# Kernel optimization log

Measured on AMD Instinct MI355X. Metric: run time of the kernel, lower is better.

The kernel has to match this reference:

```python
import jax, jax.numpy as jnp
import numpy as np

UNITS = 1024
OUT_STEPS = 200
SEQ_LEN = 5
NUM_FEATURES = 1
BATCH = 4096


def _lstm_cell(x, h, c, kernel, recurrent_kernel, bias):
    # Keras LSTMCell: z = x@K + h@R + b, gates in order i, f, g(candidate), o
    z = x @ kernel + h @ recurrent_kernel + bias  # [B, 4U]
    i, f, g, o = jnp.split(z, 4, axis=-1)
    i = jax.nn.sigmoid(i)
    f = jax.nn.sigmoid(f)
    g = jnp.tanh(g)
    o = jax.nn.sigmoid(o)
    c_new = f * c + i * g
    h_new = o * jnp.tanh(c_new)
    return h_new, c_new


def setup_inputs() -> dict:
    key = jax.random.key(0)
    ks = jax.random.split(key, 8)
    s = 0.05  # modest init scale to keep gates unsaturated
    return {
        "inputs": jax.random.normal(ks[0], (BATCH, SEQ_LEN, NUM_FEATURES), jnp.float32),
        "kernel": jax.random.normal(ks[1], (NUM_FEATURES, 4 * UNITS), jnp.float32) * s,
        "recurrent_kernel": jax.random.normal(ks[2], (UNITS, 4 * UNITS), jnp.float32) * s,
        "bias": jax.random.normal(ks[3], (4 * UNITS,), jnp.float32) * s,
        "w1": jax.random.normal(ks[4], (UNITS, NUM_FEATURES), jnp.float32) * s,
        "b1": jax.random.normal(ks[5], (NUM_FEATURES,), jnp.float32) * s,
        "w2": jax.random.normal(ks[6], (NUM_FEATURES, NUM_FEATURES), jnp.float32) * s,
        "b2": jax.random.normal(ks[7], (NUM_FEATURES,), jnp.float32) * s,
    }


def reference(inputs, kernel, recurrent_kernel, bias, w1, b1, w2, b2):
    B = inputs.shape[0]
    h0 = jnp.zeros((B, UNITS), inputs.dtype)
    c0 = jnp.zeros((B, UNITS), inputs.dtype)

    # warmup: run LSTM over the input sequence (lax.scan over time)
    def warm_step(carry, x_t):
        h, c = carry
        h, c = _lstm_cell(x_t, h, c, kernel, recurrent_kernel, bias)
        return (h, c), None

    (h, c), _ = jax.lax.scan(warm_step, (h0, c0), jnp.swapaxes(inputs, 0, 1))
    pred0 = jax.nn.relu(h @ w1 + b1)  # first prediction: dense1 only (per warmup())

    def dec_step(carry, _):
        pred, h, c = carry
        h, c = _lstm_cell(pred, h, c, kernel, recurrent_kernel, bias)
        x = jax.nn.relu(h @ w1 + b1)
        pred = x @ w2 + b2
        return (pred, h, c), pred

    _, preds = jax.lax.scan(dec_step, (pred0, h, c), None, length=OUT_STEPS - 1)
    # preds: [T-1, B, F] -> stack with pred0 and transpose to [B, T, F]
    all_preds = jnp.concatenate([pred0[None], preds], axis=0)
    return jnp.transpose(all_preds, (1, 0, 2))
```

## Files before the change

### kernel.cpp

```cpp
#include <hip/hip_runtime.h>
#include <hip/hip_bf16.h>
#include <stdint.h>
#include <stddef.h>

#define B_SZ   4096
#define U_SZ   1024
#define SEQ    5
#define TSTEPS 200
#define STEPS  204

typedef __bf16 bf16_t;
typedef __bf16 bf16x8 __attribute__((ext_vector_type(8)));
typedef float  f32x4  __attribute__((ext_vector_type(4)));

#define AS1 __attribute__((address_space(1)))
#define AS3 __attribute__((address_space(3)))

#define LOAD_LDS16(gp, lp) \
    __builtin_amdgcn_global_load_lds((const AS1 unsigned int*)(gp), \
                                     (AS3 unsigned int*)(lp), 16, 0, 0)

__device__ __forceinline__ float fsig(float x) {
    return 1.0f / (1.0f + __expf(-x));
}
__device__ __forceinline__ float ftanh(float x) {
    x = fminf(fmaxf(x, -15.0f), 15.0f);
    float e = __expf(2.0f * x);
    return (e - 1.0f) / (e + 1.0f);
}

__global__ void pack_R(const float* __restrict__ R, bf16_t* __restrict__ Rp) {
    int idx = blockIdx.x * 256 + threadIdx.x;
    int e    = idx & 7;
    int slot = (idx >> 3) & 7;
    int c    = (idx >> 6) & 127;
    int kb   = (idx >> 13) & 15;
    int ub   = idx >> 17;
    int g  = (c >> 4) & 3;
    int wc = c >> 6;
    int cl = c & 15;
    int n  = g * 1024 + ub * 32 + wc * 16 + cl;
    int k  = kb * 64 + ((slot ^ (c & 7)) << 3) + e;
    Rp[idx] = (bf16_t)R[(size_t)k * 4096 + n];
}

__global__ __launch_bounds__(256, 2)
void lstm_step(const bf16_t* __restrict__ hin,
               bf16_t* __restrict__ hout,
               float* __restrict__ cst,
               const bf16_t* __restrict__ Rp,
               const float* __restrict__ Wx,
               const float* __restrict__ bias,
               const float* __restrict__ w1,
               const float* __restrict__ b1,
               const float* __restrict__ w2,
               const float* __restrict__ b2,
               const float* __restrict__ inputs,
               float* __restrict__ praw,
               float* __restrict__ out,
               int t)
{
    __shared__ __align__(16) bf16_t lsA[128 * 64];
    __shared__ __align__(16) bf16_t lsB[2][128 * 64];
    __shared__ float lsX[128];

    const int tid  = threadIdx.x;
    const int wave = tid >> 6;
    const int lane = tid & 63;
    const int p    = blockIdx.x;
    const int G    = blockIdx.y;
    const int l15  = lane & 15;
    const int quad = lane >> 4;
    const int rbase = (wave >> 1) * 64;
    const int wc    = wave & 1;

    float*       pr_acc  = praw + (size_t)(t % 3) * B_SZ;
    const float* pr_read = praw + (size_t)((t + 2) % 3) * B_SZ;
    float*       pr_zero = praw + (size_t)((t + 1) % 3) * B_SZ;

    if (tid < 128) {
        int row = G * 128 + tid;
        float x;
        if (t < SEQ) {
            x = inputs[row * SEQ + t];
        } else {
            float x1 = fmaxf(pr_read[row] + b1[0], 0.f);
            x = (t == SEQ) ? x1 : x1 * w2[0] + b2[0];
            if (p == 0) out[(size_t)row * TSTEPS + (t - SEQ)] = x;
        }
        lsX[tid] = x;
        if (p == 0) pr_zero[row] = 0.f;
    }

    f32x4 acc[2][4][4] = {};
    const bf16_t* Ap  = hin + (size_t)G * 128 * U_SZ;
    const bf16_t* Bp0 = Rp + (size_t)(2 * p) * 131072;
    const bf16_t* Bp1 = Bp0 + 131072;

    const int a_kk = (((lane & 7) ^ (lane >> 3)) << 3);

    for (int kb = 0; kb < 16; ++kb) {
        #pragma unroll
        for (int i = 0; i < 4; ++i) {
            int chunk = wave * 4 + i;
            int m  = chunk * 8 + (lane >> 3);
            LOAD_LDS16(Ap + (size_t)m * U_SZ + kb * 64 + a_kk, &lsA[chunk * 512]);
        }
        #pragma unroll
        for (int i = 0; i < 4; ++i) {
            int chunk = wave * 4 + i;
            LOAD_LDS16(Bp0 + (size_t)kb * 8192 + chunk * 512 + lane * 8,
                       &lsB[0][chunk * 512]);
            LOAD_LDS16(Bp1 + (size_t)kb * 8192 + chunk * 512 + lane * 8,
                       &lsB[1][chunk * 512]);
        }
        __syncthreads();

        #pragma unroll
        for (int kh = 0; kh < 2; ++kh) {
            int sw = (((kh * 4 + quad) ^ (lane & 7)) << 3);
            bf16x8 af[4];
            #pragma unroll
            for (int mi = 0; mi < 4; ++mi)
                af[mi] = *(const bf16x8*)&lsA[(rbase + mi * 16 + l15) * 64 + sw];
            #pragma unroll
            for (int T = 0; T < 2; ++T) {
                bf16x8 bfr[4];
                #pragma unroll
                for (int ni = 0; ni < 4; ++ni)
                    bfr[ni] = *(const bf16x8*)
                        &lsB[T][(wc * 64 + ni * 16 + l15) * 64 + sw];
                #pragma unroll
                for (int mi = 0; mi < 4; ++mi)
                    #pragma unroll
                    for (int ni = 0; ni < 4; ++ni)
                        acc[T][mi][ni] = __builtin_amdgcn_mfma_f32_16x16x32_bf16(
                            af[mi], bfr[ni], acc[T][mi][ni], 0, 0, 0);
            }
        }
        __syncthreads();
    }

    int uu[2];
    uu[0] = (2 * p) * 32 + wc * 16 + l15;
    uu[1] = uu[0] + 32;
    float g_b[2][4], g_w[2][4], w1u[2];
    #pragma unroll
    for (int T = 0; T < 2; ++T) {
        #pragma unroll
        for (int g = 0; g < 4; ++g) {
            g_b[T][g] = bias[g * 1024 + uu[T]];
            g_w[T][g] = Wx[g * 1024 + uu[T]];
        }
        w1u[T] = w1[uu[T]];
    }
    const bool do_pred = (t >= SEQ - 1);

    #pragma unroll
    for (int mi = 0; mi < 4; ++mi) {
        #pragma unroll
        for (int r = 0; r < 4; ++r) {
            int rl   = rbase + mi * 16 + quad * 4 + r;
            int brow = G * 128 + rl;
            float xv = lsX[rl];
            float ps = 0.f;
            #pragma unroll
            for (int T = 0; T < 2; ++T) {
                float zi = acc[T][mi][0][r] + g_b[T][0] + xv * g_w[T][0];
                float zf = acc[T][mi][1][r] + g_b[T][1] + xv * g_w[T][1];
                float zg = acc[T][mi][2][r] + g_b[T][2] + xv * g_w[T][2];
                float zo = acc[T][mi][3][r] + g_b[T][3] + xv * g_w[T][3];
                float ig = fsig(zi), fg = fsig(zf);
                float gg = ftanh(zg), og = fsig(zo);
                size_t off = (size_t)brow * U_SZ + uu[T];
                float cn = fg * cst[off] + ig * gg;
                cst[off] = cn;
                float hv = og * ftanh(cn);
                hout[off] = (bf16_t)hv;
                ps += hv * w1u[T];
            }
            if (do_pred) {
                ps += __shfl_xor(ps, 1);
                ps += __shfl_xor(ps, 2);
                ps += __shfl_xor(ps, 4);
                ps += __shfl_xor(ps, 8);
                if (l15 == 0) atomicAdd(&pr_acc[brow], ps);
            }
        }
    }
}

__global__ void pred_final(const float* __restrict__ praw,
                           const float* __restrict__ b1,
                           const float* __restrict__ w2,
                           const float* __restrict__ b2,
                           float* __restrict__ out)
{
    int row = blockIdx.x * 256 + threadIdx.x;
    float x1 = fmaxf(praw[2 * B_SZ + row] + b1[0], 0.f);
    out[(size_t)row * TSTEPS + 199] = x1 * w2[0] + b2[0];
}

extern "C" void kernel_launch(void* const* d_in, const int* in_sizes, int n_in,
                              void* d_out, int out_size, void* d_ws, size_t ws_size,
                              hipStream_t stream) {
    const float* inputs = (const float*)d_in[0];
    const float* Wx     = (const float*)d_in[1];
    const float* R      = (const float*)d_in[2];
    const float* bias   = (const float*)d_in[3];
    const float* w1     = (const float*)d_in[4];
    const float* b1     = (const float*)d_in[5];
    const float* w2     = (const float*)d_in[6];
    const float* b2     = (const float*)d_in[7];
    float* out = (float*)d_out;

    char* ws = (char*)d_ws;
    const size_t RP_BYTES = (size_t)32 * 131072 * 2;
    const size_t H_BYTES  = (size_t)B_SZ * U_SZ * 2;
    const size_t C_BYTES  = (size_t)B_SZ * U_SZ * 4;
    bf16_t* Rp   = (bf16_t*)ws;                ws += RP_BYTES;
    bf16_t* h0   = (bf16_t*)ws;                ws += H_BYTES;
    bf16_t* h1   = (bf16_t*)ws;                ws += H_BYTES;
    float*  cbuf = (float*)ws;                 ws += C_BYTES;
    float*  praw = (float*)ws;                 ws += 3 * B_SZ * 4;
    bf16_t* hb[2] = {h0, h1};

    hipMemsetAsync(h0, 0, H_BYTES, stream);
    hipMemsetAsync(cbuf, 0, C_BYTES, stream);
    hipMemsetAsync(praw, 0, 3 * B_SZ * 4, stream);

    pack_R<<<16384, 256, 0, stream>>>(R, Rp);

    dim3 grid(16, 32);
    int cur = 0;
    for (int t = 0; t < STEPS; ++t) {
        lstm_step<<<grid, 256, 0, stream>>>(hb[cur], hb[1 - cur], cbuf, Rp,
                                            Wx, bias, w1, b1, w2, b2,
                                            inputs, praw, out, t);
        cur ^= 1;
    }
    pred_final<<<16, 256, 0, stream>>>(praw, b1, w2, b2, out);
}
```

Baseline: 8.692 ms.

## Replace per-step launches with persistent cooperative kernel and per-group barriers

Runs all 204 recurrent steps inside one cooperative persistent kernel. Blocks sharing a batch group synchronise through an atomic counter barrier instead of kernel boundaries. The cell state now stays on chip, half in LDS and half in registers, so it no longer round-trips through global memory. The first K-tile of the recurrent weights is prefetched for the next step during the epilogue. This removes per-launch overhead and the c-state traffic, but adds the barrier spin cost and more LDS per block, which may limit occupancy. A fallback to the old multi-launch path is kept.

```diff
diff --git a/kernel.cpp b/kernel.cpp
--- a/kernel.cpp
+++ b/kernel.cpp
@@ -8,6 +8,8 @@
 #define SEQ    5
 #define TSTEPS 200
 #define STEPS  204
+#define NP     16
+#define NG     32
 
 typedef __bf16 bf16_t;
 typedef __bf16 bf16x8 __attribute__((ext_vector_type(8)));
@@ -42,6 +44,194 @@
     int n  = g * 1024 + ub * 32 + wc * 16 + cl;
     int k  = kb * 64 + ((slot ^ (c & 7)) << 3) + e;
     Rp[idx] = (bf16_t)R[(size_t)k * 4096 + n];
+}
+
+__global__ __launch_bounds__(256, 2)
+void lstm_persist(bf16_t* __restrict__ h0,
+                  bf16_t* __restrict__ h1,
+                  const bf16_t* __restrict__ Rp,
+                  const float* __restrict__ Wx,
+                  const float* __restrict__ bias,
+                  const float* __restrict__ w1,
+                  const float* __restrict__ b1,
+                  const float* __restrict__ w2,
+                  const float* __restrict__ b2,
+                  const float* __restrict__ inputs,
+                  float* __restrict__ praw,
+                  float* __restrict__ out,
+                  unsigned int* __restrict__ bar)
+{
+    __shared__ __align__(16) bf16_t lsA[128 * 64];
+    __shared__ __align__(16) bf16_t lsB[2][128 * 64];
+    __shared__ float lsX[128];
+    __shared__ float lsC[128 * 32];
+
+    const int tid  = threadIdx.x;
+    const int wave = tid >> 6;
+    const int lane = tid & 63;
+    const int p    = blockIdx.x;
+    const int G    = blockIdx.y;
+    const int l15  = lane & 15;
+    const int quad = lane >> 4;
+    const int rbase = (wave >> 1) * 64;
+    const int wc    = wave & 1;
+    const int a_kk  = (((lane & 7) ^ (lane >> 3)) << 3);
+
+    const bf16_t* Bp0 = Rp + (size_t)(2 * p) * 131072;
+    const bf16_t* Bp1 = Bp0 + 131072;
+
+    const int uuA[2] = { (2 * p) * 32 + wc * 16 + l15,
+                         (2 * p) * 32 + wc * 16 + l15 + 32 };
+
+    const float b1s = b1[0], w2s = w2[0], b2s = b2[0];
+
+    for (int i = tid; i < 4096; i += 256) lsC[i] = 0.f;
+    float c1[4][4] = {};
+
+    #pragma clang loop unroll(disable)
+    for (int t = 0; t < STEPS; ++t) {
+        const bf16_t* hin  = (t & 1) ? h1 : h0;
+        bf16_t*       hout = (t & 1) ? h0 : h1;
+        float*       pr_acc  = praw + (size_t)(t % 3) * B_SZ;
+        const float* pr_read = praw + (size_t)((t + 2) % 3) * B_SZ;
+        float*       pr_zero = praw + (size_t)((t + 1) % 3) * B_SZ;
+
+        if (tid < 128) {
+            int row = G * 128 + tid;
+            float x;
+            if (t < SEQ) {
+                x = inputs[row * SEQ + t];
+            } else {
+                float x1 = fmaxf(pr_read[row] + b1s, 0.f);
+                x = (t == SEQ) ? x1 : x1 * w2s + b2s;
+                if (p == 0) out[(size_t)row * TSTEPS + (t - SEQ)] = x;
+            }
+            lsX[tid] = x;
+            if (p == 0) pr_zero[row] = 0.f;
+        }
+
+        f32x4 acc[2][4][4] = {};
+        const bf16_t* Ap = hin + (size_t)G * 128 * U_SZ;
+
+        for (int kb = 0; kb < 16; ++kb) {
+            #pragma unroll
+            for (int i = 0; i < 4; ++i) {
+                int chunk = wave * 4 + i;
+                int m  = chunk * 8 + (lane >> 3);
+                LOAD_LDS16(Ap + (size_t)m * U_SZ + kb * 64 + a_kk, &lsA[chunk * 512]);
+            }
+            if (kb > 0 || t == 0) {
+                #pragma unroll
+                for (int i = 0; i < 4; ++i) {
+                    int chunk = wave * 4 + i;
+                    LOAD_LDS16(Bp0 + (size_t)kb * 8192 + chunk * 512 + lane * 8,
+                               &lsB[0][chunk * 512]);
+                    LOAD_LDS16(Bp1 + (size_t)kb * 8192 + chunk * 512 + lane * 8,
+                               &lsB[1][chunk * 512]);
+                }
+            }
+            __syncthreads();
+
+            #pragma unroll
+            for (int kh = 0; kh < 2; ++kh) {
+                int sw = (((kh * 4 + quad) ^ (lane & 7)) << 3);
+                bf16x8 af[4];
+                #pragma unroll
+                for (int mi = 0; mi < 4; ++mi)
+                    af[mi] = *(const bf16x8*)&lsA[(rbase + mi * 16 + l15) * 64 + sw];
+                #pragma unroll
+                for (int T = 0; T < 2; ++T) {
+                    bf16x8 bfr[4];
+                    #pragma unroll
+                    for (int ni = 0; ni < 4; ++ni)
+                        bfr[ni] = *(const bf16x8*)
+                            &lsB[T][(wc * 64 + ni * 16 + l15) * 64 + sw];
+                    #pragma unroll
+                    for (int mi = 0; mi < 4; ++mi)
+                        #pragma unroll
+                        for (int ni = 0; ni < 4; ++ni)
+                            acc[T][mi][ni] = __builtin_amdgcn_mfma_f32_16x16x32_bf16(
+                                af[mi], bfr[ni], acc[T][mi][ni], 0, 0, 0);
+                }
+            }
+            __syncthreads();
+        }
+
+        if (t + 1 < STEPS) {
+            #pragma unroll
+            for (int i = 0; i < 4; ++i) {
+                int chunk = wave * 4 + i;
+                LOAD_LDS16(Bp0 + chunk * 512 + lane * 8, &lsB[0][chunk * 512]);
+                LOAD_LDS16(Bp1 + chunk * 512 + lane * 8, &lsB[1][chunk * 512]);
+            }
+        }
+
+        float g_b[2][4], g_w[2][4], w1u[2];
+        #pragma unroll
+        for (int T = 0; T < 2; ++T) {
+            #pragma unroll
+            for (int g = 0; g < 4; ++g) {
+                g_b[T][g] = bias[g * 1024 + uuA[T]];
+                g_w[T][g] = Wx[g * 1024 + uuA[T]];
+            }
+            w1u[T] = w1[uuA[T]];
+        }
+        const bool do_pred = (t >= SEQ - 1);
+
+        #pragma unroll
+        for (int mi = 0; mi < 4; ++mi) {
+            #pragma unroll
+            for (int r = 0; r < 4; ++r) {
+                int rl   = rbase + mi * 16 + quad * 4 + r;
+                int brow = G * 128 + rl;
+                float xv = lsX[rl];
+                int ci = rl * 32 + ((wc * 16 + l15) ^ (quad << 3));
+                float ps = 0.f;
+                #pragma unroll
+                for (int T = 0; T < 2; ++T) {
+                    float zi = acc[T][mi][0][r] + g_b[T][0] + xv * g_w[T][0];
+                    float zf = acc[T][mi][1][r] + g_b[T][1] + xv * g_w[T][1];
+                    float zg = acc[T][mi][2][r] + g_b[T][2] + xv * g_w[T][2];
+                    float zo = acc[T][mi][3][r] + g_b[T][3] + xv * g_w[T][3];
+                    float ig = fsig(zi), fg = fsig(zf);
+                    float gg = ftanh(zg), og = fsig(zo);
+                    float c_old = (T == 0) ? lsC[ci] : c1[mi][r];
+                    float cn = fg * c_old + ig * gg;
+                    if (T == 0) lsC[ci] = cn; else c1[mi][r] = cn;
+                    float hv = og * ftanh(cn);
+                    hout[(size_t)brow * U_SZ + uuA[T]] = (bf16_t)hv;
+                    ps += hv * w1u[T];
+                }
+                if (do_pred) {
+                    ps += __shfl_xor(ps, 1);
+                    ps += __shfl_xor(ps, 2);
+                    ps += __shfl_xor(ps, 4);
+                    ps += __shfl_xor(ps, 8);
+                    if (l15 == 0) atomicAdd(&pr_acc[brow], ps);
+                }
+            }
+        }
+
+        __atomic_thread_fence(__ATOMIC_RELEASE);
+        __syncthreads();
+        if (tid == 0) {
+            unsigned int* c0 = &bar[G << 5];
+            __hip_atomic_fetch_add(c0, 1u, __ATOMIC_RELAXED,
+                                   __HIP_MEMORY_SCOPE_SYSTEM);
+            const unsigned tgt = (unsigned)(NP * (t + 1));
+            while (__hip_atomic_load(c0, __ATOMIC_RELAXED,
+                                     __HIP_MEMORY_SCOPE_SYSTEM) < tgt)
+                __builtin_amdgcn_s_sleep(2);
+        }
+        __syncthreads();
+        __atomic_thread_fence(__ATOMIC_ACQUIRE);
+    }
+
+    if (p == 0 && tid < 128) {
+        int row = G * 128 + tid;
+        float x1 = fmaxf(praw[2 * B_SZ + row] + b1s, 0.f);
+        out[(size_t)row * TSTEPS + 199] = x1 * w2s + b2s;
+    }
 }
 
 __global__ __launch_bounds__(256, 2)
@@ -96,7 +286,6 @@
     const bf16_t* Ap  = hin + (size_t)G * 128 * U_SZ;
     const bf16_t* Bp0 = Rp + (size_t)(2 * p) * 131072;
     const bf16_t* Bp1 = Bp0 + 131072;
-
     const int a_kk = (((lane & 7) ^ (lane >> 3)) << 3);
 
     for (int kb = 0; kb < 16; ++kb) {
@@ -218,26 +407,49 @@
     const size_t RP_BYTES = (size_t)32 * 131072 * 2;
     const size_t H_BYTES  = (size_t)B_SZ * U_SZ * 2;
     const size_t C_BYTES  = (size_t)B_SZ * U_SZ * 4;
+    const size_t PR_BYTES = (size_t)3 * B_SZ * 4;
     bf16_t* Rp   = (bf16_t*)ws;                ws += RP_BYTES;
     bf16_t* h0   = (bf16_t*)ws;                ws += H_BYTES;
     bf16_t* h1   = (bf16_t*)ws;                ws += H_BYTES;
     float*  cbuf = (float*)ws;                 ws += C_BYTES;
-    float*  praw = (float*)ws;                 ws += 3 * B_SZ * 4;
+    float*  praw = (float*)ws;                 ws += PR_BYTES;
+    unsigned int* bar = (unsigned int*)cbuf;
     bf16_t* hb[2] = {h0, h1};
 
     hipMemsetAsync(h0, 0, H_BYTES, stream);
     hipMemsetAsync(cbuf, 0, C_BYTES, stream);
-    hipMemsetAsync(praw, 0, 3 * B_SZ * 4, stream);
+    hipMemsetAsync(praw, 0, PR_BYTES, stream);
 
     pack_R<<<16384, 256, 0, stream>>>(R, Rp);
 
-    dim3 grid(16, 32);
-    int cur = 0;
-    for (int t = 0; t < STEPS; ++t) {
-        lstm_step<<<grid, 256, 0, stream>>>(hb[cur], hb[1 - cur], cbuf, Rp,
-                                            Wx, bias, w1, b1, w2, b2,
-                                            inputs, praw, out, t);
-        cur ^= 1;
-    }
-    pred_final<<<16, 256, 0, stream>>>(praw, b1, w2, b2, out);
-}
+    void* args[13];
+    args[0]  = (void*)&h0;
+    args[1]  = (void*)&h1;
+    args[2]  = (void*)&Rp;
+    args[3]  = (void*)&Wx;
+    args[4]  = (void*)&bias;
+    args[5]  = (void*)&w1;
+    args[6]  = (void*)&b1;
+    args[7]  = (void*)&w2;
+    args[8]  = (void*)&b2;
+    args[9]  = (void*)&inputs;
+    args[10] = (void*)&praw;
+    args[11] = (void*)&out;
+    args[12] = (void*)&bar;
+
+    hipError_t cerr = hipLaunchCooperativeKernel((const void*)lstm_persist,
+                                                 dim3(NP, NG), dim3(256, 1, 1),
+                                                 args, 0, stream);
+    if (cerr != hipSuccess) {
+        (void)hipGetLastError();
+        dim3 grid(NP, NG);
+        int cur = 0;
+        for (int t = 0; t < STEPS; ++t) {
+            lstm_step<<<grid, 256, 0, stream>>>(hb[cur], hb[1 - cur], cbuf, Rp,
+                                                Wx, bias, w1, b1, w2, b2,
+                                                inputs, praw, out, t);
+            cur ^= 1;
+        }
+        pred_final<<<16, 256, 0, stream>>>(praw, b1, w2, b2, out);
+    }
+}
```

After: 22.55 ms. 2.59x slower.

## Software-pipeline K-loop with double-buffered A tile and register-staged fragments

Applied to the files above, without the earlier changes.

Double-buffers the A (hidden state) LDS tile and prefetches the next K-block's A and B tiles while MFMAs run on the current block. All fragments are read into registers before a mid-loop barrier, which frees the single B buffer to be overwritten early. MFMA issue priority is also raised with setprio. The goal is to hide global-to-LDS load latency behind compute, at the cost of more registers and reliance on manual waitcnt and barrier ordering being correct.

```diff
diff --git a/kernel.cpp b/kernel.cpp
--- a/kernel.cpp
+++ b/kernel.cpp
@@ -60,8 +60,8 @@
                float* __restrict__ out,
                int t)
 {
-    __shared__ __align__(16) bf16_t lsA[128 * 64];
-    __shared__ __align__(16) bf16_t lsB[2][128 * 64];
+    __shared__ __align__(16) bf16_t lsA[2][8192];
+    __shared__ __align__(16) bf16_t lsB[2][8192];
     __shared__ float lsX[128];
 
     const int tid  = threadIdx.x;
@@ -73,10 +73,28 @@
     const int quad = lane >> 4;
     const int rbase = (wave >> 1) * 64;
     const int wc    = wave & 1;
+    const int a_kk  = (((lane & 7) ^ (lane >> 3)) << 3);
 
     float*       pr_acc  = praw + (size_t)(t % 3) * B_SZ;
     const float* pr_read = praw + (size_t)((t + 2) % 3) * B_SZ;
     float*       pr_zero = praw + (size_t)((t + 1) % 3) * B_SZ;
+
+    const bf16_t* Ap  = hin + (size_t)G * 128 * U_SZ;
+    const bf16_t* Bp0 = Rp + (size_t)(2 * p) * 131072;
+    const bf16_t* Bp1 = Bp0 + 131072;
+
+    #pragma unroll
+    for (int i = 0; i < 4; ++i) {
+        int chunk = wave * 4 + i;
+        int m  = chunk * 8 + (lane >> 3);
+        LOAD_LDS16(Ap + (size_t)m * U_SZ + a_kk, &lsA[0][chunk * 512]);
+    }
+    #pragma unroll
+    for (int i = 0; i < 4; ++i) {
+        int chunk = wave * 4 + i;
+        LOAD_LDS16(Bp0 + chunk * 512 + lane * 8, &lsB[0][chunk * 512]);
+        LOAD_LDS16(Bp1 + chunk * 512 + lane * 8, &lsB[1][chunk * 512]);
+    }
 
     if (tid < 128) {
         int row = G * 128 + tid;
@@ -93,52 +111,66 @@
     }
 
     f32x4 acc[2][4][4] = {};
-    const bf16_t* Ap  = hin + (size_t)G * 128 * U_SZ;
-    const bf16_t* Bp0 = Rp + (size_t)(2 * p) * 131072;
-    const bf16_t* Bp1 = Bp0 + 131072;
-
-    const int a_kk = (((lane & 7) ^ (lane >> 3)) << 3);
 
     for (int kb = 0; kb < 16; ++kb) {
-        #pragma unroll
-        for (int i = 0; i < 4; ++i) {
-            int chunk = wave * 4 + i;
-            int m  = chunk * 8 + (lane >> 3);
-            LOAD_LDS16(Ap + (size_t)m * U_SZ + kb * 64 + a_kk, &lsA[chunk * 512]);
-        }
-        #pragma unroll
-        for (int i = 0; i < 4; ++i) {
-            int chunk = wave * 4 + i;
-            LOAD_LDS16(Bp0 + (size_t)kb * 8192 + chunk * 512 + lane * 8,
-                       &lsB[0][chunk * 512]);
-            LOAD_LDS16(Bp1 + (size_t)kb * 8192 + chunk * 512 + lane * 8,
-                       &lsB[1][chunk * 512]);
-        }
         __syncthreads();
 
+        if (kb < 15) {
+            const int kn = kb + 1;
+            #pragma unroll
+            for (int i = 0; i < 4; ++i) {
+                int chunk = wave * 4 + i;
+                int m  = chunk * 8 + (lane >> 3);
+                LOAD_LDS16(Ap + (size_t)m * U_SZ + kn * 64 + a_kk,
+                           &lsA[kn & 1][chunk * 512]);
+            }
+        }
+
+        const bf16_t* la = &lsA[kb & 1][0];
+        bf16x8 af[2][4], bfr[2][2][4];
         #pragma unroll
         for (int kh = 0; kh < 2; ++kh) {
             int sw = (((kh * 4 + quad) ^ (lane & 7)) << 3);
-            bf16x8 af[4];
             #pragma unroll
             for (int mi = 0; mi < 4; ++mi)
-                af[mi] = *(const bf16x8*)&lsA[(rbase + mi * 16 + l15) * 64 + sw];
-            #pragma unroll
-            for (int T = 0; T < 2; ++T) {
-                bf16x8 bfr[4];
+                af[kh][mi] = *(const bf16x8*)&la[(rbase + mi * 16 + l15) * 64 + sw];
+            #pragma unroll
+            for (int T = 0; T < 2; ++T)
                 #pragma unroll
                 for (int ni = 0; ni < 4; ++ni)
-                    bfr[ni] = *(const bf16x8*)
+                    bfr[kh][T][ni] = *(const bf16x8*)
                         &lsB[T][(wc * 64 + ni * 16 + l15) * 64 + sw];
+        }
+
+        asm volatile("s_waitcnt lgkmcnt(0)" ::: "memory");
+        __builtin_amdgcn_sched_barrier(0);
+        __builtin_amdgcn_s_barrier();
+        __builtin_amdgcn_sched_barrier(0);
+
+        if (kb < 15) {
+            const int kn = kb + 1;
+            #pragma unroll
+            for (int i = 0; i < 4; ++i) {
+                int chunk = wave * 4 + i;
+                LOAD_LDS16(Bp0 + (size_t)kn * 8192 + chunk * 512 + lane * 8,
+                           &lsB[0][chunk * 512]);
+                LOAD_LDS16(Bp1 + (size_t)kn * 8192 + chunk * 512 + lane * 8,
+                           &lsB[1][chunk * 512]);
+            }
+        }
+
+        __builtin_amdgcn_s_setprio(1);
+        #pragma unroll
+        for (int kh = 0; kh < 2; ++kh)
+            #pragma unroll
+            for (int T = 0; T < 2; ++T)
                 #pragma unroll
                 for (int mi = 0; mi < 4; ++mi)
                     #pragma unroll
                     for (int ni = 0; ni < 4; ++ni)
                         acc[T][mi][ni] = __builtin_amdgcn_mfma_f32_16x16x32_bf16(
-                            af[mi], bfr[ni], acc[T][mi][ni], 0, 0, 0);
-            }
-        }
-        __syncthreads();
+                            af[kh][mi], bfr[kh][T][ni], acc[T][mi][ni], 0, 0, 0);
+        __builtin_amdgcn_s_setprio(0);
     }
 
     int uu[2];
```

After: 8.638 ms. Within noise of the previous version (-0.6%).

## Triple-buffer LDS K-tiles with prefetch two ahead and one barrier per step

Applied to the files above, without the earlier changes.

The K loop now uses 32-wide K tiles instead of 64-wide, held in three LDS buffers. Loads for tile kb+2 are issued while tile kb is computed, with a partial vmcnt wait and a single barrier per iteration, and the packed R layout and swizzle are changed to match. This is meant to hide global-to-LDS load latency behind MFMA work, replacing the load-then-sync-then-compute pattern. It also raises MFMA priority with setprio. The extra prefetches at the tail wrap around and reload tiles 0 and 1, which is redundant traffic. The ring reuses a buffer only after the barrier, so the ordering relies on the vmcnt(6) accounting being right.

```diff
diff --git a/kernel.cpp b/kernel.cpp
--- a/kernel.cpp
+++ b/kernel.cpp
@@ -32,15 +32,15 @@
 __global__ void pack_R(const float* __restrict__ R, bf16_t* __restrict__ Rp) {
     int idx = blockIdx.x * 256 + threadIdx.x;
     int e    = idx & 7;
-    int slot = (idx >> 3) & 7;
-    int c    = (idx >> 6) & 127;
-    int kb   = (idx >> 13) & 15;
+    int slot = (idx >> 3) & 3;
+    int c    = (idx >> 5) & 127;
+    int kb   = (idx >> 12) & 31;
     int ub   = idx >> 17;
     int g  = (c >> 4) & 3;
     int wc = c >> 6;
     int cl = c & 15;
     int n  = g * 1024 + ub * 32 + wc * 16 + cl;
-    int k  = kb * 64 + ((slot ^ (c & 7)) << 3) + e;
+    int k  = kb * 32 + ((slot ^ ((c >> 1) & 3)) << 3) + e;
     Rp[idx] = (bf16_t)R[(size_t)k * 4096 + n];
 }
 
@@ -60,8 +60,8 @@
                float* __restrict__ out,
                int t)
 {
-    __shared__ __align__(16) bf16_t lsA[128 * 64];
-    __shared__ __align__(16) bf16_t lsB[2][128 * 64];
+    __shared__ __align__(16) bf16_t lsA[3][4096];
+    __shared__ __align__(16) bf16_t lsB[3][2][4096];
     __shared__ float lsX[128];
 
     const int tid  = threadIdx.x;
@@ -73,10 +73,16 @@
     const int quad = lane >> 4;
     const int rbase = (wave >> 1) * 64;
     const int wc    = wave & 1;
+    const int a_kk32 = (((lane & 3) ^ ((lane >> 3) & 3)) << 3);
+    const int sw32   = ((quad ^ ((l15 >> 1) & 3)) << 3);
 
     float*       pr_acc  = praw + (size_t)(t % 3) * B_SZ;
     const float* pr_read = praw + (size_t)((t + 2) % 3) * B_SZ;
     float*       pr_zero = praw + (size_t)((t + 1) % 3) * B_SZ;
+
+    const bf16_t* Ap  = hin + (size_t)G * 128 * U_SZ;
+    const bf16_t* Bp0 = Rp + (size_t)(2 * p) * 131072;
+    const bf16_t* Bp1 = Bp0 + 131072;
 
     if (tid < 128) {
         int row = G * 128 + tid;
@@ -92,53 +98,63 @@
         if (p == 0) pr_zero[row] = 0.f;
     }
 
+    auto STAGE = [&](int ksrc, int buf) {
+        #pragma unroll
+        for (int i = 0; i < 2; ++i) {
+            int brow = i * 64 + wave * 16;
+            LOAD_LDS16(Ap + (size_t)(brow + (lane >> 2)) * U_SZ
+                          + ksrc * 32 + a_kk32,
+                       &lsA[buf][brow * 32]);
+        }
+        #pragma unroll
+        for (int i = 0; i < 2; ++i) {
+            int chunk = wave * 2 + i;
+            LOAD_LDS16(Bp0 + (size_t)ksrc * 4096 + chunk * 512 + lane * 8,
+                       &lsB[buf][0][chunk * 512]);
+            LOAD_LDS16(Bp1 + (size_t)ksrc * 4096 + chunk * 512 + lane * 8,
+                       &lsB[buf][1][chunk * 512]);
+        }
+    };
+
+    STAGE(0, 0);
+    STAGE(1, 1);
+
     f32x4 acc[2][4][4] = {};
-    const bf16_t* Ap  = hin + (size_t)G * 128 * U_SZ;
-    const bf16_t* Bp0 = Rp + (size_t)(2 * p) * 131072;
-    const bf16_t* Bp1 = Bp0 + 131072;
-
-    const int a_kk = (((lane & 7) ^ (lane >> 3)) << 3);
-
-    for (int kb = 0; kb < 16; ++kb) {
-        #pragma unroll
-        for (int i = 0; i < 4; ++i) {
-            int chunk = wave * 4 + i;
-            int m  = chunk * 8 + (lane >> 3);
-            LOAD_LDS16(Ap + (size_t)m * U_SZ + kb * 64 + a_kk, &lsA[chunk * 512]);
-        }
-        #pragma unroll
-        for (int i = 0; i < 4; ++i) {
-            int chunk = wave * 4 + i;
-            LOAD_LDS16(Bp0 + (size_t)kb * 8192 + chunk * 512 + lane * 8,
-                       &lsB[0][chunk * 512]);
-            LOAD_LDS16(Bp1 + (size_t)kb * 8192 + chunk * 512 + lane * 8,
-                       &lsB[1][chunk * 512]);
-        }
-        __syncthreads();
-
-        #pragma unroll
-        for (int kh = 0; kh < 2; ++kh) {
-            int sw = (((kh * 4 + quad) ^ (lane & 7)) << 3);
-            bf16x8 af[4];
+    int bi = 0;
+
+    for (int kb = 0; kb < 32; ++kb) {
+        asm volatile("s_waitcnt vmcnt(6)" ::: "memory");
+        __builtin_amdgcn_sched_barrier(0);
+        __builtin_amdgcn_s_barrier();
+        __builtin_amdgcn_sched_barrier(0);
+
+        int bs = bi + 2; if (bs >= 3) bs -= 3;
+        STAGE((kb + 2) & 31, bs);
+
+        bf16x8 af[4], bfr[2][4];
+        #pragma unroll
+        for (int mi = 0; mi < 4; ++mi)
+            af[mi] = *(const bf16x8*)
+                &lsA[bi][(rbase + mi * 16 + l15) * 32 + sw32];
+        #pragma unroll
+        for (int T = 0; T < 2; ++T)
+            #pragma unroll
+            for (int ni = 0; ni < 4; ++ni)
+                bfr[T][ni] = *(const bf16x8*)
+                    &lsB[bi][T][(wc * 64 + ni * 16 + l15) * 32 + sw32];
+
+        __builtin_amdgcn_s_setprio(1);
+        #pragma unroll
+        for (int T = 0; T < 2; ++T)
             #pragma unroll
             for (int mi = 0; mi < 4; ++mi)
-                af[mi] = *(const bf16x8*)&lsA[(rbase + mi * 16 + l15) * 64 + sw];
-            #pragma unroll
-            for (int T = 0; T < 2; ++T) {
-                bf16x8 bfr[4];
                 #pragma unroll
                 for (int ni = 0; ni < 4; ++ni)
-                    bfr[ni] = *(const bf16x8*)
-                        &lsB[T][(wc * 64 + ni * 16 + l15) * 64 + sw];
-                #pragma unroll
-                for (int mi = 0; mi < 4; ++mi)
-                    #pragma unroll
-                    for (int ni = 0; ni < 4; ++ni)
-                        acc[T][mi][ni] = __builtin_amdgcn_mfma_f32_16x16x32_bf16(
-                            af[mi], bfr[ni], acc[T][mi][ni], 0, 0, 0);
-            }
-        }
-        __syncthreads();
+                    acc[T][mi][ni] = __builtin_amdgcn_mfma_f32_16x16x32_bf16(
+                        af[mi], bfr[T][ni], acc[T][mi][ni], 0, 0, 0);
+        __builtin_amdgcn_s_setprio(0);
+
+        bi = bi + 1; if (bi >= 3) bi = 0;
     }
 
     int uu[2];
```

After: 9.719 ms. 1.12x slower.
